# Optimization experiments

Hardware: AMD Instinct MI355X
Metric: run time of the kernel (lower is better)

## Reference

```python
import jax, jax.numpy as jnp
import numpy as np

HIDDEN = 1024
INTER = 4096
EPS = 1e-12


def _ste(q, x):
    # straight-through estimator: forward q, backward identity wrt x
    return x + jax.lax.stop_gradient(q - x)


def setup_inputs() -> dict:
    key = jax.random.key(0)
    ks = jax.random.split(key, 4)
    hidden_states = jax.random.normal(ks[0], (4, 2048, INTER), dtype=jnp.float32)
    input_tensor = jax.random.normal(ks[1], (4, 2048, HIDDEN), dtype=jnp.float32)
    W = jax.random.normal(ks[2], (HIDDEN, INTER), dtype=jnp.float32) * 0.02
    b = jnp.zeros((HIDDEN,), dtype=jnp.float32)
    clip_val = jnp.asarray(2.5, dtype=jnp.float32)  # learnable elastic alpha
    gamma = jnp.ones((HIDDEN,), dtype=jnp.float32)
    beta = jnp.zeros((HIDDEN,), dtype=jnp.float32)
    return {"hidden_states": hidden_states, "input_tensor": input_tensor,
            "W": W, "b": b, "clip_val": clip_val, "gamma": gamma, "beta": beta}


def reference(hidden_states, input_tensor, W, b, clip_val, gamma, beta):
    # --- binary weight (BWN): per-output-channel scale = mean(|W|, axis=in) ---
    w_scale = jnp.mean(jnp.abs(W), axis=1, keepdims=True)  # [hidden, 1]
    W_q = _ste(w_scale * jnp.sign(W), W)                    # [hidden, inter]
    # --- elastic signed binary activation: q = alpha * sign(x / alpha) ---
    s = hidden_states / clip_val
    x_q = clip_val * _ste(jnp.sign(s), s)                   # [b, s, inter]
    # --- dense projection ---
    h = jnp.einsum('bsi,hi->bsh', x_q, W_q) + b             # [b, s, hidden]
    # dropout prob 0.0 (eval mode) -> no-op
    # --- residual + LayerNorm (eps=1e-12) ---
    r = h + input_tensor
    mu = jnp.mean(r, axis=-1, keepdims=True)
    var = jnp.mean(jnp.square(r - mu), axis=-1, keepdims=True)
    out = (r - mu) * jax.lax.rsqrt(var + EPS) * gamma + beta
    return out
```

## Files before the change

kernel.cpp:

```cpp
#include <hip/hip_runtime.h>
#include <stdint.h>

#define HIDDEN 1024
#define INTER  4096
#define NWORDS 64
#define ROWS   8192
#define MT     16

typedef unsigned long long u64;

__global__ __launch_bounds__(256)
void pack_a_kernel(const float* __restrict__ hs, u64* __restrict__ abits) {
    int m    = blockIdx.x;
    int lane = threadIdx.x & 63;
    int wave = threadIdx.x >> 6;
    const float* row = hs + (size_t)m * INTER;
    for (int w = wave; w < NWORDS; w += 4) {
        float x  = row[w * 64 + lane];
        u64 mask = __ballot(x < 0.0f);
        if (lane == 0) abits[(size_t)m * NWORDS + w] = mask;
    }
}

__global__ __launch_bounds__(256)
void pack_w_kernel(const float* __restrict__ W, u64* __restrict__ wbits_t,
                   float* __restrict__ wscale) {
    int h    = blockIdx.x;
    int lane = threadIdx.x & 63;
    int wave = threadIdx.x >> 6;
    const float* row = W + (size_t)h * INTER;
    float asum = 0.f;
    for (int w = wave; w < NWORDS; w += 4) {
        float x = row[w * 64 + lane];
        asum += fabsf(x);
        u64 mask = __ballot(x < 0.0f);
        if (lane == 0) wbits_t[w * HIDDEN + h] = mask;
    }
    #pragma unroll
    for (int off = 32; off > 0; off >>= 1) asum += __shfl_down(asum, off);
    __shared__ float red[4];
    if (lane == 0) red[wave] = asum;
    __syncthreads();
    if (threadIdx.x == 0) {
        float total = red[0] + red[1] + red[2] + red[3];
        wscale[h] = total * (1.0f / INTER);
    }
}

__global__ __launch_bounds__(256)
void gemm_ln_kernel(const u64* __restrict__ abits, const u64* __restrict__ wbits_t,
                    const float* __restrict__ wscale, const float* __restrict__ bias,
                    const float* __restrict__ clipp, const float* __restrict__ input,
                    const float* __restrict__ gamma, const float* __restrict__ beta,
                    float* __restrict__ out) {
    int m0 = blockIdx.x * MT;
    int t  = threadIdx.x;

    __shared__ u64 sA[MT * NWORDS];
    const u64* ap = abits + (size_t)m0 * NWORDS;
    for (int i = t; i < MT * NWORDS; i += 256) sA[i] = ap[i];
    __syncthreads();

    int h0 = t * 4;
    int acc[MT][4];
    #pragma unroll
    for (int mi = 0; mi < MT; ++mi)
        #pragma unroll
        for (int hh = 0; hh < 4; ++hh) acc[mi][hh] = 0;

    #pragma unroll 2
    for (int k = 0; k < NWORDS; ++k) {
        const u64* wp = wbits_t + (size_t)k * HIDDEN + h0;
        u64 b0 = wp[0];
        u64 b1 = wp[1];
        u64 b2 = wp[2];
        u64 b3 = wp[3];
        #pragma unroll
        for (int mi = 0; mi < MT; ++mi) {
            u64 a = sA[mi * NWORDS + k];
            acc[mi][0] += __popcll(a ^ b0);
            acc[mi][1] += __popcll(a ^ b1);
            acc[mi][2] += __popcll(a ^ b2);
            acc[mi][3] += __popcll(a ^ b3);
        }
    }

    float clip = clipp[0];
    float4 cw = reinterpret_cast<const float4*>(wscale)[t];
    cw.x *= clip; cw.y *= clip; cw.z *= clip; cw.w *= clip;
    float4 bi = reinterpret_cast<const float4*>(bias)[t];
    float4 gm = reinterpret_cast<const float4*>(gamma)[t];
    float4 bt = reinterpret_cast<const float4*>(beta)[t];

    float vals[MT][4];
    #pragma unroll
    for (int mi = 0; mi < MT; ++mi) {
        float4 inp = reinterpret_cast<const float4*>(input + (size_t)(m0 + mi) * HIDDEN)[t];
        vals[mi][0] = fmaf((float)(INTER - 2 * acc[mi][0]), cw.x, bi.x + inp.x);
        vals[mi][1] = fmaf((float)(INTER - 2 * acc[mi][1]), cw.y, bi.y + inp.y);
        vals[mi][2] = fmaf((float)(INTER - 2 * acc[mi][2]), cw.z, bi.z + inp.z);
        vals[mi][3] = fmaf((float)(INTER - 2 * acc[mi][3]), cw.w, bi.w + inp.w);
    }

    __shared__ float red_s[4][MT];
    __shared__ float red_q[4][MT];
    __shared__ float s_mu[MT], s_rs[MT];
    int lane = t & 63, wave = t >> 6;
    #pragma unroll
    for (int mi = 0; mi < MT; ++mi) {
        float s = vals[mi][0] + vals[mi][1] + vals[mi][2] + vals[mi][3];
        float q = vals[mi][0] * vals[mi][0] + vals[mi][1] * vals[mi][1]
                + vals[mi][2] * vals[mi][2] + vals[mi][3] * vals[mi][3];
        #pragma unroll
        for (int off = 32; off > 0; off >>= 1) {
            s += __shfl_down(s, off);
            q += __shfl_down(q, off);
        }
        if (lane == 0) { red_s[wave][mi] = s; red_q[wave][mi] = q; }
    }
    __syncthreads();
    if (t < MT) {
        float s = red_s[0][t] + red_s[1][t] + red_s[2][t] + red_s[3][t];
        float q = red_q[0][t] + red_q[1][t] + red_q[2][t] + red_q[3][t];
        float mu  = s * (1.0f / HIDDEN);
        float var = fmaf(-mu, mu, q * (1.0f / HIDDEN));
        s_mu[t] = mu;
        s_rs[t] = rsqrtf(var + 1e-12f);
    }
    __syncthreads();

    #pragma unroll
    for (int mi = 0; mi < MT; ++mi) {
        float mu = s_mu[mi], rs = s_rs[mi];
        float4 o;
        o.x = (vals[mi][0] - mu) * rs * gm.x + bt.x;
        o.y = (vals[mi][1] - mu) * rs * gm.y + bt.y;
        o.z = (vals[mi][2] - mu) * rs * gm.z + bt.z;
        o.w = (vals[mi][3] - mu) * rs * gm.w + bt.w;
        reinterpret_cast<float4*>(out + (size_t)(m0 + mi) * HIDDEN)[t] = o;
    }
}

extern "C" void kernel_launch(void* const* d_in, const int* in_sizes, int n_in,
                              void* d_out, int out_size, void* d_ws, size_t ws_size,
                              hipStream_t stream) {
    const float* hs    = (const float*)d_in[0];
    const float* inp   = (const float*)d_in[1];
    const float* W     = (const float*)d_in[2];
    const float* b     = (const float*)d_in[3];
    const float* clip  = (const float*)d_in[4];
    const float* gamma = (const float*)d_in[5];
    const float* beta  = (const float*)d_in[6];
    float* out = (float*)d_out;

    u64*   abits  = (u64*)d_ws;
    u64*   wbits  = (u64*)((char*)d_ws + (size_t)ROWS * NWORDS * 8);
    float* wscale = (float*)((char*)d_ws + (size_t)ROWS * NWORDS * 8
                                         + (size_t)NWORDS * HIDDEN * 8);

    pack_a_kernel<<<ROWS, 256, 0, stream>>>(hs, abits);
    pack_w_kernel<<<HIDDEN, 256, 0, stream>>>(W, wbits, wscale);
    gemm_ln_kernel<<<ROWS / MT, 256, 0, stream>>>(abits, wbits, wscale, b, clip,
                                                  inp, gamma, beta, out);
}
```

Measured before the change: 340.9 us.

## Merge pack kernels, tile-major activation bits, drop LDS staging, halve row tile

Combines the activation and weight bit-packing kernels into one launch, with each wave packing a whole activation row. The packed activation bits are written in a tile-interleaved layout so the GEMM reads them directly from global memory as uniform broadcast loads instead of staging through shared memory with a barrier. The row tile per block is halved to 8 and launch bounds request 4 blocks per SM, trading weight-bit reuse per block for lower register pressure and higher occupancy. Global weight loads are now amortized over fewer rows, which adds L2 traffic.

```diff
diff --git a/kernel.cpp b/kernel.cpp
--- a/kernel.cpp
+++ b/kernel.cpp
@@ -5,83 +5,81 @@
 #define INTER  4096
 #define NWORDS 64
 #define ROWS   8192
-#define MT     16
+#define MT     8
+#define GBLK   (ROWS / MT)
 
 typedef unsigned long long u64;
 
 __global__ __launch_bounds__(256)
-void pack_a_kernel(const float* __restrict__ hs, u64* __restrict__ abits) {
-    int m    = blockIdx.x;
+void pack_kernel(const float* __restrict__ hs, const float* __restrict__ W,
+                 u64* __restrict__ abits_t, u64* __restrict__ wbits_t,
+                 float* __restrict__ wscale) {
     int lane = threadIdx.x & 63;
     int wave = threadIdx.x >> 6;
-    const float* row = hs + (size_t)m * INTER;
-    for (int w = wave; w < NWORDS; w += 4) {
-        float x  = row[w * 64 + lane];
-        u64 mask = __ballot(x < 0.0f);
-        if (lane == 0) abits[(size_t)m * NWORDS + w] = mask;
+    int b = blockIdx.x;
+
+    if (b < ROWS / 4) {
+        int m = b * 4 + wave;
+        const float* row = hs + (size_t)m * INTER;
+        u64* dst = abits_t + (size_t)(m >> 3) * NWORDS * MT + (m & 7);
+        #pragma unroll 4
+        for (int w = 0; w < NWORDS; ++w) {
+            float x = row[w * 64 + lane];
+            u64 mask = __ballot(x < 0.0f);
+            if (lane == 0) dst[(size_t)w * MT] = mask;
+        }
+    } else {
+        int h = b - ROWS / 4;
+        const float* row = W + (size_t)h * INTER;
+        float asum = 0.f;
+        for (int w = wave; w < NWORDS; w += 4) {
+            float x = row[w * 64 + lane];
+            asum += fabsf(x);
+            u64 mask = __ballot(x < 0.0f);
+            if (lane == 0) wbits_t[(size_t)w * HIDDEN + h] = mask;
+        }
+        #pragma unroll
+        for (int off = 32; off > 0; off >>= 1) asum += __shfl_down(asum, off);
+        __shared__ float red[4];
+        if (lane == 0) red[wave] = asum;
+        __syncthreads();
+        if (threadIdx.x == 0)
+            wscale[h] = (red[0] + red[1] + red[2] + red[3]) * (1.0f / INTER);
     }
 }
 
-__global__ __launch_bounds__(256)
-void pack_w_kernel(const float* __restrict__ W, u64* __restrict__ wbits_t,
-                   float* __restrict__ wscale) {
-    int h    = blockIdx.x;
-    int lane = threadIdx.x & 63;
-    int wave = threadIdx.x >> 6;
-    const float* row = W + (size_t)h * INTER;
-    float asum = 0.f;
-    for (int w = wave; w < NWORDS; w += 4) {
-        float x = row[w * 64 + lane];
-        asum += fabsf(x);
-        u64 mask = __ballot(x < 0.0f);
-        if (lane == 0) wbits_t[w * HIDDEN + h] = mask;
-    }
-    #pragma unroll
-    for (int off = 32; off > 0; off >>= 1) asum += __shfl_down(asum, off);
-    __shared__ float red[4];
-    if (lane == 0) red[wave] = asum;
-    __syncthreads();
-    if (threadIdx.x == 0) {
-        float total = red[0] + red[1] + red[2] + red[3];
-        wscale[h] = total * (1.0f / INTER);
-    }
-}
-
-__global__ __launch_bounds__(256)
-void gemm_ln_kernel(const u64* __restrict__ abits, const u64* __restrict__ wbits_t,
+__global__ __launch_bounds__(256, 4)
+void gemm_ln_kernel(const u64* __restrict__ abits_t, const u64* __restrict__ wbits_t,
                     const float* __restrict__ wscale, const float* __restrict__ bias,
                     const float* __restrict__ clipp, const float* __restrict__ input,
                     const float* __restrict__ gamma, const float* __restrict__ beta,
                     float* __restrict__ out) {
+    int t  = threadIdx.x;
     int m0 = blockIdx.x * MT;
-    int t  = threadIdx.x;
+    int h0 = t * 4;
+    const u64* ablk = abits_t + (size_t)blockIdx.x * NWORDS * MT;
 
-    __shared__ u64 sA[MT * NWORDS];
-    const u64* ap = abits + (size_t)m0 * NWORDS;
-    for (int i = t; i < MT * NWORDS; i += 256) sA[i] = ap[i];
-    __syncthreads();
-
-    int h0 = t * 4;
     int acc[MT][4];
     #pragma unroll
     for (int mi = 0; mi < MT; ++mi)
         #pragma unroll
-        for (int hh = 0; hh < 4; ++hh) acc[mi][hh] = 0;
+        for (int c = 0; c < 4; ++c) acc[mi][c] = 0;
 
     #pragma unroll 2
     for (int k = 0; k < NWORDS; ++k) {
         const u64* wp = wbits_t + (size_t)k * HIDDEN + h0;
-        u64 b0 = wp[0];
-        u64 b1 = wp[1];
-        u64 b2 = wp[2];
-        u64 b3 = wp[3];
+        u64 w0 = wp[0];
+        u64 w1 = wp[1];
+        u64 w2 = wp[2];
+        u64 w3 = wp[3];
+        const u64* ap = ablk + k * MT;
         #pragma unroll
         for (int mi = 0; mi < MT; ++mi) {
-            u64 a = sA[mi * NWORDS + k];
-            acc[mi][0] += __popcll(a ^ b0);
-            acc[mi][1] += __popcll(a ^ b1);
-            acc[mi][2] += __popcll(a ^ b2);
-            acc[mi][3] += __popcll(a ^ b3);
+            u64 a = ap[mi];
+            acc[mi][0] += __popcll(a ^ w0);
+            acc[mi][1] += __popcll(a ^ w1);
+            acc[mi][2] += __popcll(a ^ w2);
+            acc[mi][3] += __popcll(a ^ w3);
         }
     }
 
@@ -158,8 +156,7 @@
     float* wscale = (float*)((char*)d_ws + (size_t)ROWS * NWORDS * 8
                                          + (size_t)NWORDS * HIDDEN * 8);
 
-    pack_a_kernel<<<ROWS, 256, 0, stream>>>(hs, abits);
-    pack_w_kernel<<<HIDDEN, 256, 0, stream>>>(W, wbits, wscale);
-    gemm_ln_kernel<<<ROWS / MT, 256, 0, stream>>>(abits, wbits, wscale, b, clip,
-                                                  inp, gamma, beta, out);
+    pack_kernel<<<ROWS / 4 + HIDDEN, 256, 0, stream>>>(hs, W, abits, wbits, wscale);
+    gemm_ln_kernel<<<GBLK, 256, 0, stream>>>(abits, wbits, wscale, b, clip,
+                                             inp, gamma, beta, out);
 }
```

New measurement: 333.7 us. -2.1%, faster.
